# Performance work log

Hardware: AMD Instinct MI355X
Metric: run time of the kernel (lower is better)

The kernel has to match this reference:

```python
import jax, jax.numpy as jnp
import numpy as np

K = 20  # neighbors


def _knn_idx(x, k):
    # x: (B, N, C). pairwise_distance[b,i,j] = -||x_i - x_j||^2; topk -> k nearest (incl. self)
    inner = jnp.einsum('bic,bjc->bij', x, x)            # (B, N, N)
    sq = jnp.sum(x * x, axis=-1)                         # (B, N)
    pd = 2.0 * inner - sq[:, :, None] - sq[:, None, :]   # (B, N, N)
    return jax.lax.top_k(pd, k)[1]                       # (B, N, k) int32


def _gather_neighbors(x, idx):
    # Faithful to source: flatten to (B*N, C) and index with per-batch indices in [0, N).
    # This means every batch gathers from batch 0's rows (bug in original, reproduced).
    B, N, C = x.shape
    flat = x.reshape(B * N, C)
    return flat[idx.reshape(-1)].reshape(B, N, idx.shape[-1], C)  # (B, N, k, C)


def setup_inputs() -> dict:
    key = jax.random.key(0)
    ks = jax.random.split(key, 11)
    B, N = 8, 4096
    emb_dim = 1024
    s = 0.05
    inp = {
        'x':  jax.random.normal(ks[0], (B, N, 3), dtype=jnp.float32),
        'w1': jax.random.normal(ks[1], (3, 64), dtype=jnp.float32) * s,
        'b1': jax.random.normal(ks[2], (64,), dtype=jnp.float32) * s,
        'w2': jax.random.normal(ks[3], (64, 64), dtype=jnp.float32) * s,
        'b2': jax.random.normal(ks[4], (64,), dtype=jnp.float32) * s,
        'w3': jax.random.normal(ks[5], (64, 64), dtype=jnp.float32) * s,
        'b3': jax.random.normal(ks[6], (64,), dtype=jnp.float32) * s,
        'w4': jax.random.normal(ks[7], (64, 128), dtype=jnp.float32) * s,
        'b4': jax.random.normal(ks[8], (128,), dtype=jnp.float32) * s,
        'w5': jax.random.normal(ks[9], (128, emb_dim), dtype=jnp.float32) * s,
        'b5': jax.random.normal(ks[10], (emb_dim,), dtype=jnp.float32) * s,
    }
    return inp


def reference(x, w1, b1, w2, b2, w3, b3, w4, b4, w5, b5):
    # Stage 1: knn on xyz, gather, mlp1 (3->64->64->64 with ReLUs), max over k
    idx = _knn_idx(x, K)                                  # (B, N, K)
    nb = _gather_neighbors(x, idx)                        # (B, N, K, 3)
    h = jax.nn.relu(nb @ w1 + b1)
    h = jax.nn.relu(h @ w2 + b2)
    h = h @ w3 + b3                                       # (B, N, K, 64)
    h = jnp.max(h, axis=2)                                # (B, N, 64)
    # Stage 2: knn on 64-d features, gather, mlp2 (64->128), max over k
    idx = _knn_idx(h, K)
    nb = _gather_neighbors(h, idx)                        # (B, N, K, 64)
    h = nb @ w4 + b4                                      # (B, N, K, 128)
    h = jnp.max(h, axis=2)                                # (B, N, 128)
    # mlp3 (128 -> emb_dim)
    return h @ w5 + b5                                    # (B, N, emb_dim)
```

## Files before the change

kernel.cpp:

```cpp
#include <hip/hip_runtime.h>
#include <stddef.h>

#define NBATCH 8
#define NP 4096
#define KNN 20
#define NEGF (-3.402823466e38f)


template<int G>
__device__ __forceinline__ void knn1_group(const float* __restrict__ xb,
                                           const float* __restrict__ sqb,
                                           int lane, float xi0, float xi1, float xi2,
                                           unsigned mask8, float& gmv, int& gmt) {
  const float* xg = xb + 3 * ((lane << 6) | (G * 8));
  const float* sg = sqb + ((lane << 6) | (G * 8));
  float4 v0 = *(const float4*)(xg + 0);
  float4 v1 = *(const float4*)(xg + 4);
  float4 v2 = *(const float4*)(xg + 8);
  float4 v3 = *(const float4*)(xg + 12);
  float4 v4 = *(const float4*)(xg + 16);
  float4 v5 = *(const float4*)(xg + 20);
  float4 s0 = *(const float4*)(sg + 0);
  float4 s1 = *(const float4*)(sg + 4);
  float d0 = fmaf(xi2, v0.z, fmaf(xi1, v0.y, xi0 * v0.x)); d0 = fmaf(d0, 2.f, -s0.x);
  float d1 = fmaf(xi2, v1.y, fmaf(xi1, v1.x, xi0 * v0.w)); d1 = fmaf(d1, 2.f, -s0.y);
  float d2 = fmaf(xi2, v2.x, fmaf(xi1, v1.w, xi0 * v1.z)); d2 = fmaf(d2, 2.f, -s0.z);
  float d3 = fmaf(xi2, v2.w, fmaf(xi1, v2.z, xi0 * v2.y)); d3 = fmaf(d3, 2.f, -s0.w);
  float d4 = fmaf(xi2, v3.z, fmaf(xi1, v3.y, xi0 * v3.x)); d4 = fmaf(d4, 2.f, -s1.x);
  float d5 = fmaf(xi2, v4.y, fmaf(xi1, v4.x, xi0 * v3.w)); d5 = fmaf(d5, 2.f, -s1.y);
  float d6 = fmaf(xi2, v5.x, fmaf(xi1, v4.w, xi0 * v4.z)); d6 = fmaf(d6, 2.f, -s1.z);
  float d7 = fmaf(xi2, v5.w, fmaf(xi1, v5.z, xi0 * v5.y)); d7 = fmaf(d7, 2.f, -s1.w);
  if (mask8 & 1u)   d0 = NEGF;
  if (mask8 & 2u)   d1 = NEGF;
  if (mask8 & 4u)   d2 = NEGF;
  if (mask8 & 8u)   d3 = NEGF;
  if (mask8 & 16u)  d4 = NEGF;
  if (mask8 & 32u)  d5 = NEGF;
  if (mask8 & 64u)  d6 = NEGF;
  if (mask8 & 128u) d7 = NEGF;
  float mv = d0; int mt = 0;
  if (d1 > mv) { mv = d1; mt = 1; }
  if (d2 > mv) { mv = d2; mt = 2; }
  if (d3 > mv) { mv = d3; mt = 3; }
  if (d4 > mv) { mv = d4; mt = 4; }
  if (d5 > mv) { mv = d5; mt = 5; }
  if (d6 > mv) { mv = d6; mt = 6; }
  if (d7 > mv) { mv = d7; mt = 7; }
  gmv = mv; gmt = G * 8 + mt;
}

template<int G>
__device__ __forceinline__ void sel_group(const float* __restrict__ prow,
                                          unsigned mask8, float& gmv, int& gmt) {
  float4 a = *(const float4*)(prow + G * 8);
  float4 b = *(const float4*)(prow + G * 8 + 4);
  float d0 = a.x, d1 = a.y, d2 = a.z, d3 = a.w;
  float d4 = b.x, d5 = b.y, d6 = b.z, d7 = b.w;
  if (mask8 & 1u)   d0 = NEGF;
  if (mask8 & 2u)   d1 = NEGF;
  if (mask8 & 4u)   d2 = NEGF;
  if (mask8 & 8u)   d3 = NEGF;
  if (mask8 & 16u)  d4 = NEGF;
  if (mask8 & 32u)  d5 = NEGF;
  if (mask8 & 64u)  d6 = NEGF;
  if (mask8 & 128u) d7 = NEGF;
  float mv = d0; int mt = 0;
  if (d1 > mv) { mv = d1; mt = 1; }
  if (d2 > mv) { mv = d2; mt = 2; }
  if (d3 > mv) { mv = d3; mt = 3; }
  if (d4 > mv) { mv = d4; mt = 4; }
  if (d5 > mv) { mv = d5; mt = 5; }
  if (d6 > mv) { mv = d6; mt = 6; }
  if (d7 > mv) { mv = d7; mt = 7; }
  gmv = mv; gmt = G * 8 + mt;
}

#define LANE_SCAN()                                            \
  lv = gv0; lt = gt0;                                          \
  if (gv1 > lv) { lv = gv1; lt = gt1; }                        \
  if (gv2 > lv) { lv = gv2; lt = gt2; }                        \
  if (gv3 > lv) { lv = gv3; lt = gt3; }                        \
  if (gv4 > lv) { lv = gv4; lt = gt4; }                        \
  if (gv5 > lv) { lv = gv5; lt = gt5; }                        \
  if (gv6 > lv) { lv = gv6; lt = gt6; }                        \
  if (gv7 > lv) { lv = gv7; lt = gt7; }

__global__ __launch_bounds__(256) void sq_kernel(const float* __restrict__ x,
                                                 float* __restrict__ sqx) {
  int gid = blockIdx.x * 256 + threadIdx.x;
  float a = x[gid * 3 + 0];
  float b = x[gid * 3 + 1];
  float c = x[gid * 3 + 2];
  sqx[gid] = a * a + b * b + c * c;
}

__global__ __launch_bounds__(256) void knn1_kernel(const float* __restrict__ x,
                                                   const float* __restrict__ sqx,
                                                   int* __restrict__ idx1) {
  int wave = threadIdx.x >> 6, lane = threadIdx.x & 63;
  int row = blockIdx.x * 4 + wave;
  int b = row >> 12;
  int i = row & (NP - 1);
  const float* xb = x + (size_t)b * NP * 3;
  const float* sqb = sqx + b * NP;
  float xi0 = xb[i * 3 + 0], xi1 = xb[i * 3 + 1], xi2 = xb[i * 3 + 2];

  float gv0, gv1, gv2, gv3, gv4, gv5, gv6, gv7;
  int   gt0, gt1, gt2, gt3, gt4, gt5, gt6, gt7;
  unsigned rm0 = 0u, rm1 = 0u;
  knn1_group<0>(xb, sqb, lane, xi0, xi1, xi2, 0u, gv0, gt0);
  knn1_group<1>(xb, sqb, lane, xi0, xi1, xi2, 0u, gv1, gt1);
  knn1_group<2>(xb, sqb, lane, xi0, xi1, xi2, 0u, gv2, gt2);
  knn1_group<3>(xb, sqb, lane, xi0, xi1, xi2, 0u, gv3, gt3);
  knn1_group<4>(xb, sqb, lane, xi0, xi1, xi2, 0u, gv4, gt4);
  knn1_group<5>(xb, sqb, lane, xi0, xi1, xi2, 0u, gv5, gt5);
  knn1_group<6>(xb, sqb, lane, xi0, xi1, xi2, 0u, gv6, gt6);
  knn1_group<7>(xb, sqb, lane, xi0, xi1, xi2, 0u, gv7, gt7);
  float lv; int lt;
  LANE_SCAN();

  int myidx = 0;
  #pragma unroll 1
  for (int r = 0; r < KNN; ++r) {
    float mv = lv;
    int mj = (lane << 6) | lt;
    #pragma unroll
    for (int off = 32; off; off >>= 1) {
      float om = __shfl_xor(mv, off, 64);
      int   oj = __shfl_xor(mj, off, 64);
      if (om > mv || (om == mv && oj < mj)) { mv = om; mj = oj; }
    }
    if (lane == r) myidx = mj;
    int mju = __builtin_amdgcn_readfirstlane(mj);
    int wl = mju >> 6, tu = mju & 63;
    if (lane == wl) {
      switch (tu >> 3) {
        case 0: rm0 |= 1u << (tu & 7);        knn1_group<0>(xb, sqb, lane, xi0, xi1, xi2, rm0 & 0xffu,         gv0, gt0); break;
        case 1: rm0 |= 1u << (8 + (tu & 7));  knn1_group<1>(xb, sqb, lane, xi0, xi1, xi2, (rm0 >> 8) & 0xffu,  gv1, gt1); break;
        case 2: rm0 |= 1u << (16 + (tu & 7)); knn1_group<2>(xb, sqb, lane, xi0, xi1, xi2, (rm0 >> 16) & 0xffu, gv2, gt2); break;
        case 3: rm0 |= 1u << (24 + (tu & 7)); knn1_group<3>(xb, sqb, lane, xi0, xi1, xi2, (rm0 >> 24) & 0xffu, gv3, gt3); break;
        case 4: rm1 |= 1u << (tu & 7);        knn1_group<4>(xb, sqb, lane, xi0, xi1, xi2, rm1 & 0xffu,         gv4, gt4); break;
        case 5: rm1 |= 1u << (8 + (tu & 7));  knn1_group<5>(xb, sqb, lane, xi0, xi1, xi2, (rm1 >> 8) & 0xffu,  gv5, gt5); break;
        case 6: rm1 |= 1u << (16 + (tu & 7)); knn1_group<6>(xb, sqb, lane, xi0, xi1, xi2, (rm1 >> 16) & 0xffu, gv6, gt6); break;
        case 7: rm1 |= 1u << (24 + (tu & 7)); knn1_group<7>(xb, sqb, lane, xi0, xi1, xi2, (rm1 >> 24) & 0xffu, gv7, gt7); break;
      }
      LANE_SCAN();
    }
  }
  if (lane < KNN) idx1[(size_t)row * KNN + lane] = myidx;
}

__global__ __launch_bounds__(256) void mlp1_kernel(const float* __restrict__ x,
                                                   const float* __restrict__ w1, const float* __restrict__ b1,
                                                   const float* __restrict__ w2, const float* __restrict__ b2,
                                                   const float* __restrict__ w3, const float* __restrict__ b3,
                                                   float* __restrict__ F1) {
  int wave = threadIdx.x >> 6, lane = threadIdx.x & 63;
  int j = blockIdx.x * 4 + wave;
  float x0 = x[j * 3 + 0], x1 = x[j * 3 + 1], x2 = x[j * 3 + 2];
  float h1 = fmaf(x2, w1[128 + lane], fmaf(x1, w1[64 + lane], fmaf(x0, w1[lane], b1[lane])));
  h1 = fmaxf(h1, 0.f);
  float acc = b2[lane];
  #pragma unroll
  for (int c = 0; c < 64; ++c) acc = fmaf(__shfl(h1, c, 64), w2[c * 64 + lane], acc);
  float h2 = fmaxf(acc, 0.f);
  acc = b3[lane];
  #pragma unroll
  for (int c = 0; c < 64; ++c) acc = fmaf(__shfl(h2, c, 64), w3[c * 64 + lane], acc);
  F1[j * 64 + lane] = acc;
}

__global__ __launch_bounds__(256) void pool1_kernel(const float* __restrict__ F1,
                                                    const int* __restrict__ idx1,
                                                    float* __restrict__ h,
                                                    float* __restrict__ sqh) {
  int wave = threadIdx.x >> 6, lane = threadIdx.x & 63;
  int row = blockIdx.x * 4 + wave;
  float m = NEGF;
  #pragma unroll
  for (int k = 0; k < KNN; ++k) {
    int jj = idx1[(size_t)row * KNN + k];
    m = fmaxf(m, F1[jj * 64 + lane]);
  }
  h[(size_t)row * 64 + lane] = m;
  float s = m * m;
  #pragma unroll
  for (int off = 32; off; off >>= 1) s += __shfl_xor(s, off, 64);
  if (lane == 0) sqh[row] = s;
}

__device__ __forceinline__ int swz(int g, int r) { return g ^ ((r & 15) ^ ((r >> 4) & 3)); }

__global__ __launch_bounds__(256) void pd_gemm_kernel(const float* __restrict__ h,
                                                      const float* __restrict__ sqh,
                                                      float* __restrict__ pd, int b) {
  __shared__ float As[64 * 64];
  __shared__ float Bs[64 * 64];
  const int it = blockIdx.x >> 6;
  const int jt = blockIdx.x & 63;
  const int i0 = it * 64, j0 = jt * 64;
  const float* hb = h + (size_t)b * NP * 64;
  const int tid = threadIdx.x;
  #pragma unroll
  for (int s = 0; s < 4; ++s) {
    int f4 = tid + s * 256;
    int r = f4 >> 4, g = f4 & 15;
    int gs = swz(g, r);
    float4 va = *reinterpret_cast<const float4*>(&hb[(size_t)(i0 + r) * 64 + g * 4]);
    *reinterpret_cast<float4*>(&As[r * 64 + gs * 4]) = va;
    float4 vb = *reinterpret_cast<const float4*>(&hb[(size_t)(j0 + r) * 64 + g * 4]);
    *reinterpret_cast<float4*>(&Bs[r * 64 + gs * 4]) = vb;
  }
  __syncthreads();
  const int tx = tid & 15, ty = tid >> 4;
  float acc[4][4] = {};
  #pragma unroll
  for (int c = 0; c < 64; c += 4) {
    int g = c >> 2;
    float4 a[4], bb[4];
    #pragma unroll
    for (int q = 0; q < 4; ++q) {
      int r = ty * 4 + q;
      a[q] = *reinterpret_cast<const float4*>(&As[r * 64 + (swz(g, r) << 2)]);
    }
    #pragma unroll
    for (int p = 0; p < 4; ++p) {
      int r = tx * 4 + p;
      bb[p] = *reinterpret_cast<const float4*>(&Bs[r * 64 + (swz(g, r) << 2)]);
    }
    #pragma unroll
    for (int q = 0; q < 4; ++q) {
      #pragma unroll
      for (int p = 0; p < 4; ++p) {
        acc[q][p] = fmaf(a[q].x, bb[p].x, acc[q][p]);
        acc[q][p] = fmaf(a[q].y, bb[p].y, acc[q][p]);
        acc[q][p] = fmaf(a[q].z, bb[p].z, acc[q][p]);
        acc[q][p] = fmaf(a[q].w, bb[p].w, acc[q][p]);
      }
    }
  }
  const float* sq = sqh + b * NP;
  float sj0 = sq[j0 + tx * 4 + 0];
  float sj1 = sq[j0 + tx * 4 + 1];
  float sj2 = sq[j0 + tx * 4 + 2];
  float sj3 = sq[j0 + tx * 4 + 3];
  #pragma unroll
  for (int q = 0; q < 4; ++q) {
    int i = i0 + ty * 4 + q;
    float sqi = sq[i];
    float4 o;
    o.x = 2.f * acc[q][0] - sqi - sj0;
    o.y = 2.f * acc[q][1] - sqi - sj1;
    o.z = 2.f * acc[q][2] - sqi - sj2;
    o.w = 2.f * acc[q][3] - sqi - sj3;
    *reinterpret_cast<float4*>(&pd[(size_t)i * NP + j0 + tx * 4]) = o;
  }
}

__global__ __launch_bounds__(256) void knn_select_kernel(const float* __restrict__ pd,
                                                         int* __restrict__ idx2, int b) {
  int wave = threadIdx.x >> 6, lane = threadIdx.x & 63;
  int row = blockIdx.x * 4 + wave;
  const float* prow = pd + (size_t)row * NP + (lane << 6);

  float gv0, gv1, gv2, gv3, gv4, gv5, gv6, gv7;
  int   gt0, gt1, gt2, gt3, gt4, gt5, gt6, gt7;
  unsigned rm0 = 0u, rm1 = 0u;
  sel_group<0>(prow, 0u, gv0, gt0);
  sel_group<1>(prow, 0u, gv1, gt1);
  sel_group<2>(prow, 0u, gv2, gt2);
  sel_group<3>(prow, 0u, gv3, gt3);
  sel_group<4>(prow, 0u, gv4, gt4);
  sel_group<5>(prow, 0u, gv5, gt5);
  sel_group<6>(prow, 0u, gv6, gt6);
  sel_group<7>(prow, 0u, gv7, gt7);
  float lv; int lt;
  LANE_SCAN();

  int myidx = 0;
  #pragma unroll 1
  for (int r = 0; r < KNN; ++r) {
    float mv = lv;
    int mj = (lane << 6) | lt;
    #pragma unroll
    for (int off = 32; off; off >>= 1) {
      float om = __shfl_xor(mv, off, 64);
      int   oj = __shfl_xor(mj, off, 64);
      if (om > mv || (om == mv && oj < mj)) { mv = om; mj = oj; }
    }
    if (lane == r) myidx = mj;
    int mju = __builtin_amdgcn_readfirstlane(mj);
    int wl = mju >> 6, tu = mju & 63;
    if (lane == wl) {
      switch (tu >> 3) {
        case 0: rm0 |= 1u << (tu & 7);        sel_group<0>(prow, rm0 & 0xffu,         gv0, gt0); break;
        case 1: rm0 |= 1u << (8 + (tu & 7));  sel_group<1>(prow, (rm0 >> 8) & 0xffu,  gv1, gt1); break;
        case 2: rm0 |= 1u << (16 + (tu & 7)); sel_group<2>(prow, (rm0 >> 16) & 0xffu, gv2, gt2); break;
        case 3: rm0 |= 1u << (24 + (tu & 7)); sel_group<3>(prow, (rm0 >> 24) & 0xffu, gv3, gt3); break;
        case 4: rm1 |= 1u << (tu & 7);        sel_group<4>(prow, rm1 & 0xffu,         gv4, gt4); break;
        case 5: rm1 |= 1u << (8 + (tu & 7));  sel_group<5>(prow, (rm1 >> 8) & 0xffu,  gv5, gt5); break;
        case 6: rm1 |= 1u << (16 + (tu & 7)); sel_group<6>(prow, (rm1 >> 16) & 0xffu, gv6, gt6); break;
        case 7: rm1 |= 1u << (24 + (tu & 7)); sel_group<7>(prow, (rm1 >> 24) & 0xffu, gv7, gt7); break;
      }
      LANE_SCAN();
    }
  }
  if (lane < KNN) idx2[(size_t)(b * NP + row) * KNN + lane] = myidx;
}

__device__ __forceinline__ void clear_slot_fb(float (&val)[64], int tw, int lw, int lane) {
  switch (tw) {
#define CS(T) case T: if (lane == lw) val[T] = NEGF; break;
    CS(0) CS(1) CS(2) CS(3) CS(4) CS(5) CS(6) CS(7)
    CS(8) CS(9) CS(10) CS(11) CS(12) CS(13) CS(14) CS(15)
    CS(16) CS(17) CS(18) CS(19) CS(20) CS(21) CS(22) CS(23)
    CS(24) CS(25) CS(26) CS(27) CS(28) CS(29) CS(30) CS(31)
    CS(32) CS(33) CS(34) CS(35) CS(36) CS(37) CS(38) CS(39)
    CS(40) CS(41) CS(42) CS(43) CS(44) CS(45) CS(46) CS(47)
    CS(48) CS(49) CS(50) CS(51) CS(52) CS(53) CS(54) CS(55)
    CS(56) CS(57) CS(58) CS(59) CS(60) CS(61) CS(62) CS(63)
#undef CS
  }
}

__device__ __forceinline__ void wave_topk_fb(float (&val)[64], int lane, int rowbase,
                                             int* __restrict__ idx_out) {
  int myidx = 0;
  #pragma unroll 1
  for (int r = 0; r < KNN; ++r) {
    float m[4]; int mt[4];
    #pragma unroll
    for (int q = 0; q < 4; ++q) { m[q] = val[q]; mt[q] = q; }
    #pragma unroll
    for (int t = 4; t < 64; t += 4) {
      #pragma unroll
      for (int q = 0; q < 4; ++q) {
        if (val[t + q] > m[q]) { m[q] = val[t + q]; mt[q] = t + q; }
      }
    }
    if (m[1] > m[0] || (m[1] == m[0] && mt[1] < mt[0])) { m[0] = m[1]; mt[0] = mt[1]; }
    if (m[3] > m[2] || (m[3] == m[2] && mt[3] < mt[2])) { m[2] = m[3]; mt[2] = mt[3]; }
    if (m[2] > m[0] || (m[2] == m[0] && mt[2] < mt[0])) { m[0] = m[2]; mt[0] = mt[2]; }
    float mv = m[0];
    int mj = mt[0] * 64 + lane;
    #pragma unroll
    for (int off = 32; off; off >>= 1) {
      float om = __shfl_xor(mv, off, 64);
      int   oj = __shfl_xor(mj, off, 64);
      if (om > mv || (om == mv && oj < mj)) { mv = om; mj = oj; }
    }
    clear_slot_fb(val, mj >> 6, mj & 63, lane);
    if (lane == r) myidx = mj;
  }
  if (lane < KNN) idx_out[(size_t)rowbase * KNN + lane] = myidx;
}

__global__ __launch_bounds__(512) void knn2_fused_kernel(const float* __restrict__ h,
                                                         const float* __restrict__ sqh,
                                                         int* __restrict__ idx2) {
  __shared__ float tile[64 * 64];
  const int wave = threadIdx.x >> 6, lane = threadIdx.x & 63;
  const int row = blockIdx.x * 8 + wave;
  const int b = row >> 12;
  const int jb = b * NP;
  float hi[64];
  #pragma unroll
  for (int q2 = 0; q2 < 16; ++q2) {
    float4 v = *reinterpret_cast<const float4*>(&h[(size_t)row * 64 + q2 * 4]);
    hi[q2 * 4 + 0] = v.x; hi[q2 * 4 + 1] = v.y; hi[q2 * 4 + 2] = v.z; hi[q2 * 4 + 3] = v.w;
  }
  float sqi = sqh[row];
  float val[64];
  #pragma unroll
  for (int tt = 0; tt < 64; ++tt) {
    __syncthreads();
    #pragma unroll
    for (int s = 0; s < 2; ++s) {
      int f4 = threadIdx.x + s * 512;
      int jj = f4 >> 4, g = f4 & 15;
      float4 v = *reinterpret_cast<const float4*>(&h[(size_t)(jb + tt * 64 + jj) * 64 + g * 4]);
      int gs = g ^ (jj & 15);
      *reinterpret_cast<float4*>(&tile[jj * 64 + gs * 4]) = v;
    }
    __syncthreads();
    float acc = 0.f;
    #pragma unroll
    for (int g = 0; g < 16; ++g) {
      int gs = g ^ (lane & 15);
      float4 v = *reinterpret_cast<const float4*>(&tile[lane * 64 + gs * 4]);
      acc = fmaf(hi[4 * g + 0], v.x, acc);
      acc = fmaf(hi[4 * g + 1], v.y, acc);
      acc = fmaf(hi[4 * g + 2], v.z, acc);
      acc = fmaf(hi[4 * g + 3], v.w, acc);
    }
    val[tt] = 2.f * acc - sqi - sqh[jb + tt * 64 + lane];
  }
  wave_topk_fb(val, lane, row, idx2);
}

__global__ __launch_bounds__(128) void g4_kernel(const float* __restrict__ h,
                                                 const float* __restrict__ w4,
                                                 const float* __restrict__ b4,
                                                 float* __restrict__ G4) {
  __shared__ float hj[64];
  int j = blockIdx.x;
  int o = threadIdx.x;
  if (o < 64) hj[o] = h[(size_t)j * 64 + o];
  __syncthreads();
  float acc = b4[o];
  #pragma unroll
  for (int c = 0; c < 64; ++c) acc = fmaf(hj[c], w4[c * 128 + o], acc);
  G4[(size_t)j * 128 + o] = acc;
}

__global__ __launch_bounds__(256) void pool2_kernel(const float* __restrict__ G4,
                                                    const int* __restrict__ idx2,
                                                    float* __restrict__ h2) {
  int gid = blockIdx.x * 256 + threadIdx.x;
  int row = gid >> 7, o = gid & 127;
  float m = NEGF;
  #pragma unroll
  for (int k = 0; k < KNN; ++k) {
    int jj = idx2[(size_t)row * KNN + k];
    m = fmaxf(m, G4[(size_t)jj * 128 + o]);
  }
  h2[(size_t)gid] = m;
}

__global__ __launch_bounds__(256) void final_gemm_kernel(const float* __restrict__ h2,
                                                         const float* __restrict__ w5,
                                                         const float* __restrict__ b5,
                                                         float* __restrict__ out) {
  __shared__ float As[64 * 128];
  __shared__ float Bs[128 * 64];
  const int mt = blockIdx.x >> 4;
  const int nt = blockIdx.x & 15;
  const int row0 = mt * 64, col0 = nt * 64;
  const int tid = threadIdx.x;
  #pragma unroll
  for (int s = 0; s < 8; ++s) {
    int f4 = tid + s * 256;
    int i = f4 >> 5, kf = f4 & 31;
    float4 v = *reinterpret_cast<const float4*>(&h2[(size_t)(row0 + i) * 128 + kf * 4]);
    *reinterpret_cast<float4*>(&As[i * 128 + kf * 4]) = v;
  }
  #pragma unroll
  for (int s = 0; s < 8; ++s) {
    int f4 = tid + s * 256;
    int k = f4 >> 4, g = f4 & 15;
    float4 v = *reinterpret_cast<const float4*>(&w5[(size_t)k * 1024 + col0 + g * 4]);
    *reinterpret_cast<float4*>(&Bs[k * 64 + g * 4]) = v;
  }
  __syncthreads();
  const int tx = tid & 15, ty = tid >> 4;
  float acc[4][4] = {};
  #pragma unroll
  for (int k = 0; k < 128; k += 4) {
    float4 a[4], bb[4];
    #pragma unroll
    for (int q = 0; q < 4; ++q)
      a[q] = *reinterpret_cast<const float4*>(&As[(ty * 4 + q) * 128 + k]);
    #pragma unroll
    for (int kk = 0; kk < 4; ++kk)
      bb[kk] = *reinterpret_cast<const float4*>(&Bs[(k + kk) * 64 + tx * 4]);
    #pragma unroll
    for (int q = 0; q < 4; ++q) {
      acc[q][0] = fmaf(a[q].w, bb[3].x, fmaf(a[q].z, bb[2].x, fmaf(a[q].y, bb[1].x, fmaf(a[q].x, bb[0].x, acc[q][0]))));
      acc[q][1] = fmaf(a[q].w, bb[3].y, fmaf(a[q].z, bb[2].y, fmaf(a[q].y, bb[1].y, fmaf(a[q].x, bb[0].y, acc[q][1]))));
      acc[q][2] = fmaf(a[q].w, bb[3].z, fmaf(a[q].z, bb[2].z, fmaf(a[q].y, bb[1].z, fmaf(a[q].x, bb[0].z, acc[q][2]))));
      acc[q][3] = fmaf(a[q].w, bb[3].w, fmaf(a[q].z, bb[2].w, fmaf(a[q].y, bb[1].w, fmaf(a[q].x, bb[0].w, acc[q][3]))));
    }
  }
  float b0 = b5[col0 + tx * 4 + 0];
  float b1 = b5[col0 + tx * 4 + 1];
  float b2 = b5[col0 + tx * 4 + 2];
  float b3 = b5[col0 + tx * 4 + 3];
  #pragma unroll
  for (int q = 0; q < 4; ++q) {
    float4 o;
    o.x = acc[q][0] + b0;
    o.y = acc[q][1] + b1;
    o.z = acc[q][2] + b2;
    o.w = acc[q][3] + b3;
    *reinterpret_cast<float4*>(&out[(size_t)(row0 + ty * 4 + q) * 1024 + col0 + tx * 4]) = o;
  }
}

extern "C" void kernel_launch(void* const* d_in, const int* in_sizes, int n_in,
                              void* d_out, int out_size, void* d_ws, size_t ws_size,
                              hipStream_t stream) {
  const float* x  = (const float*)d_in[0];
  const float* w1 = (const float*)d_in[1];
  const float* b1 = (const float*)d_in[2];
  const float* w2 = (const float*)d_in[3];
  const float* b2 = (const float*)d_in[4];
  const float* w3 = (const float*)d_in[5];
  const float* b3 = (const float*)d_in[6];
  const float* w4 = (const float*)d_in[7];
  const float* b4 = (const float*)d_in[8];
  const float* w5 = (const float*)d_in[9];
  const float* b5 = (const float*)d_in[10];
  float* out = (float*)d_out;
  char* ws = (char*)d_ws;

  float* h    = (float*)(ws + 0);
  float* sqh  = (float*)(ws + 8388608);
  int*   idx2 = (int*)  (ws + 8519680);
  char*  X    = ws + 11141120;
  float* sqx  = (float*)(X + 0);
  int*   idx1 = (int*)  (X + 131072);
  float* F1   = (float*)(X + 2752512);
  float* pd   = (float*)(X + 0);
  float* G4   = (float*)(X + 0);
  float* h2   = (float*)(X + 2097152);

  const size_t NEED_FAST = 11141120 + 67108864;

  sq_kernel<<<128, 256, 0, stream>>>(x, sqx);
  knn1_kernel<<<8192, 256, 0, stream>>>(x, sqx, idx1);
  mlp1_kernel<<<1024, 256, 0, stream>>>(x, w1, b1, w2, b2, w3, b3, F1);
  pool1_kernel<<<8192, 256, 0, stream>>>(F1, idx1, h, sqh);

  if (ws_size >= NEED_FAST) {
    for (int b = 0; b < NBATCH; ++b) {
      pd_gemm_kernel<<<4096, 256, 0, stream>>>(h, sqh, pd, b);
      knn_select_kernel<<<1024, 256, 0, stream>>>(pd, idx2, b);
    }
  } else {
    knn2_fused_kernel<<<4096, 512, 0, stream>>>(h, sqh, idx2);
  }

  g4_kernel<<<4096, 128, 0, stream>>>(h, w4, b4, G4);
  pool2_kernel<<<16384, 256, 0, stream>>>(G4, idx2, h2);
  final_gemm_kernel<<<8192, 256, 0, stream>>>(h2, w5, b5, out);
}
```

Before: 1.182 ms.

## Batch pairwise-distance and select kernels across all batches; use DPP wave max

Adds a path that, when the workspace is large enough, computes the pairwise-distance matrices for all 8 batches in one launch and runs top-k selection for all rows in a second launch. This replaces the 16 per-batch launches and their small-grid tails. Separately, the per-round argmax in both top-k loops becomes a DPP float max plus a ballot and readlane, replacing the shuffle-based value/index butterfly. The batched path needs 512MB of workspace and writes all distance matrices to memory, so it only runs if the harness provides that much.

```diff
diff --git a/kernel.cpp b/kernel.cpp
--- a/kernel.cpp
+++ b/kernel.cpp
@@ -5,6 +5,23 @@
 #define NP 4096
 #define KNN 20
 #define NEGF (-3.402823466e38f)
+
+__device__ __forceinline__ float wave_max_f32(float v) {
+  int b = __float_as_int(v), t;
+  t = __builtin_amdgcn_update_dpp(b, b, 0xB1, 0xf, 0xf, false);
+  b = __float_as_int(fmaxf(__int_as_float(b), __int_as_float(t)));
+  t = __builtin_amdgcn_update_dpp(b, b, 0x4E, 0xf, 0xf, false);
+  b = __float_as_int(fmaxf(__int_as_float(b), __int_as_float(t)));
+  t = __builtin_amdgcn_update_dpp(b, b, 0x124, 0xf, 0xf, false);
+  b = __float_as_int(fmaxf(__int_as_float(b), __int_as_float(t)));
+  t = __builtin_amdgcn_update_dpp(b, b, 0x128, 0xf, 0xf, false);
+  b = __float_as_int(fmaxf(__int_as_float(b), __int_as_float(t)));
+  t = __builtin_amdgcn_update_dpp(b, b, 0x142, 0xa, 0xf, false);
+  b = __float_as_int(fmaxf(__int_as_float(b), __int_as_float(t)));
+  t = __builtin_amdgcn_update_dpp(b, b, 0x143, 0xc, 0xf, false);
+  b = __float_as_int(fmaxf(__int_as_float(b), __int_as_float(t)));
+  return __int_as_float(__builtin_amdgcn_readlane(b, 63));
+}
 
 
 template<int G>
@@ -122,27 +139,21 @@
   int myidx = 0;
   #pragma unroll 1
   for (int r = 0; r < KNN; ++r) {
-    float mv = lv;
-    int mj = (lane << 6) | lt;
-    #pragma unroll
-    for (int off = 32; off; off >>= 1) {
-      float om = __shfl_xor(mv, off, 64);
-      int   oj = __shfl_xor(mj, off, 64);
-      if (om > mv || (om == mv && oj < mj)) { mv = om; mj = oj; }
-    }
-    if (lane == r) myidx = mj;
-    int mju = __builtin_amdgcn_readfirstlane(mj);
-    int wl = mju >> 6, tu = mju & 63;
+    float m = wave_max_f32(lv);
+    unsigned long long bal = __ballot(lv == m);
+    int wl = (int)__builtin_ctzll(bal);
+    int tsel = __builtin_amdgcn_readlane(lt, wl);
+    if (lane == r) myidx = (wl << 6) | tsel;
     if (lane == wl) {
-      switch (tu >> 3) {
-        case 0: rm0 |= 1u << (tu & 7);        knn1_group<0>(xb, sqb, lane, xi0, xi1, xi2, rm0 & 0xffu,         gv0, gt0); break;
-        case 1: rm0 |= 1u << (8 + (tu & 7));  knn1_group<1>(xb, sqb, lane, xi0, xi1, xi2, (rm0 >> 8) & 0xffu,  gv1, gt1); break;
-        case 2: rm0 |= 1u << (16 + (tu & 7)); knn1_group<2>(xb, sqb, lane, xi0, xi1, xi2, (rm0 >> 16) & 0xffu, gv2, gt2); break;
-        case 3: rm0 |= 1u << (24 + (tu & 7)); knn1_group<3>(xb, sqb, lane, xi0, xi1, xi2, (rm0 >> 24) & 0xffu, gv3, gt3); break;
-        case 4: rm1 |= 1u << (tu & 7);        knn1_group<4>(xb, sqb, lane, xi0, xi1, xi2, rm1 & 0xffu,         gv4, gt4); break;
-        case 5: rm1 |= 1u << (8 + (tu & 7));  knn1_group<5>(xb, sqb, lane, xi0, xi1, xi2, (rm1 >> 8) & 0xffu,  gv5, gt5); break;
-        case 6: rm1 |= 1u << (16 + (tu & 7)); knn1_group<6>(xb, sqb, lane, xi0, xi1, xi2, (rm1 >> 16) & 0xffu, gv6, gt6); break;
-        case 7: rm1 |= 1u << (24 + (tu & 7)); knn1_group<7>(xb, sqb, lane, xi0, xi1, xi2, (rm1 >> 24) & 0xffu, gv7, gt7); break;
+      switch (tsel >> 3) {
+        case 0: rm0 |= 1u << (tsel & 7);        knn1_group<0>(xb, sqb, lane, xi0, xi1, xi2, rm0 & 0xffu,         gv0, gt0); break;
+        case 1: rm0 |= 1u << (8 + (tsel & 7));  knn1_group<1>(xb, sqb, lane, xi0, xi1, xi2, (rm0 >> 8) & 0xffu,  gv1, gt1); break;
+        case 2: rm0 |= 1u << (16 + (tsel & 7)); knn1_group<2>(xb, sqb, lane, xi0, xi1, xi2, (rm0 >> 16) & 0xffu, gv2, gt2); break;
+        case 3: rm0 |= 1u << (24 + (tsel & 7)); knn1_group<3>(xb, sqb, lane, xi0, xi1, xi2, (rm0 >> 24) & 0xffu, gv3, gt3); break;
+        case 4: rm1 |= 1u << (tsel & 7);        knn1_group<4>(xb, sqb, lane, xi0, xi1, xi2, rm1 & 0xffu,         gv4, gt4); break;
+        case 5: rm1 |= 1u << (8 + (tsel & 7));  knn1_group<5>(xb, sqb, lane, xi0, xi1, xi2, (rm1 >> 8) & 0xffu,  gv5, gt5); break;
+        case 6: rm1 |= 1u << (16 + (tsel & 7)); knn1_group<6>(xb, sqb, lane, xi0, xi1, xi2, (rm1 >> 16) & 0xffu, gv6, gt6); break;
+        case 7: rm1 |= 1u << (24 + (tsel & 7)); knn1_group<7>(xb, sqb, lane, xi0, xi1, xi2, (rm1 >> 24) & 0xffu, gv7, gt7); break;
       }
       LANE_SCAN();
     }
@@ -150,119 +161,8 @@
   if (lane < KNN) idx1[(size_t)row * KNN + lane] = myidx;
 }
 
-__global__ __launch_bounds__(256) void mlp1_kernel(const float* __restrict__ x,
-                                                   const float* __restrict__ w1, const float* __restrict__ b1,
-                                                   const float* __restrict__ w2, const float* __restrict__ b2,
-                                                   const float* __restrict__ w3, const float* __restrict__ b3,
-                                                   float* __restrict__ F1) {
-  int wave = threadIdx.x >> 6, lane = threadIdx.x & 63;
-  int j = blockIdx.x * 4 + wave;
-  float x0 = x[j * 3 + 0], x1 = x[j * 3 + 1], x2 = x[j * 3 + 2];
-  float h1 = fmaf(x2, w1[128 + lane], fmaf(x1, w1[64 + lane], fmaf(x0, w1[lane], b1[lane])));
-  h1 = fmaxf(h1, 0.f);
-  float acc = b2[lane];
-  #pragma unroll
-  for (int c = 0; c < 64; ++c) acc = fmaf(__shfl(h1, c, 64), w2[c * 64 + lane], acc);
-  float h2 = fmaxf(acc, 0.f);
-  acc = b3[lane];
-  #pragma unroll
-  for (int c = 0; c < 64; ++c) acc = fmaf(__shfl(h2, c, 64), w3[c * 64 + lane], acc);
-  F1[j * 64 + lane] = acc;
-}
-
-__global__ __launch_bounds__(256) void pool1_kernel(const float* __restrict__ F1,
-                                                    const int* __restrict__ idx1,
-                                                    float* __restrict__ h,
-                                                    float* __restrict__ sqh) {
-  int wave = threadIdx.x >> 6, lane = threadIdx.x & 63;
-  int row = blockIdx.x * 4 + wave;
-  float m = NEGF;
-  #pragma unroll
-  for (int k = 0; k < KNN; ++k) {
-    int jj = idx1[(size_t)row * KNN + k];
-    m = fmaxf(m, F1[jj * 64 + lane]);
-  }
-  h[(size_t)row * 64 + lane] = m;
-  float s = m * m;
-  #pragma unroll
-  for (int off = 32; off; off >>= 1) s += __shfl_xor(s, off, 64);
-  if (lane == 0) sqh[row] = s;
-}
-
-__device__ __forceinline__ int swz(int g, int r) { return g ^ ((r & 15) ^ ((r >> 4) & 3)); }
-
-__global__ __launch_bounds__(256) void pd_gemm_kernel(const float* __restrict__ h,
-                                                      const float* __restrict__ sqh,
-                                                      float* __restrict__ pd, int b) {
-  __shared__ float As[64 * 64];
-  __shared__ float Bs[64 * 64];
-  const int it = blockIdx.x >> 6;
-  const int jt = blockIdx.x & 63;
-  const int i0 = it * 64, j0 = jt * 64;
-  const float* hb = h + (size_t)b * NP * 64;
-  const int tid = threadIdx.x;
-  #pragma unroll
-  for (int s = 0; s < 4; ++s) {
-    int f4 = tid + s * 256;
-    int r = f4 >> 4, g = f4 & 15;
-    int gs = swz(g, r);
-    float4 va = *reinterpret_cast<const float4*>(&hb[(size_t)(i0 + r) * 64 + g * 4]);
-    *reinterpret_cast<float4*>(&As[r * 64 + gs * 4]) = va;
-    float4 vb = *reinterpret_cast<const float4*>(&hb[(size_t)(j0 + r) * 64 + g * 4]);
-    *reinterpret_cast<float4*>(&Bs[r * 64 + gs * 4]) = vb;
-  }
-  __syncthreads();
-  const int tx = tid & 15, ty = tid >> 4;
-  float acc[4][4] = {};
-  #pragma unroll
-  for (int c = 0; c < 64; c += 4) {
-    int g = c >> 2;
-    float4 a[4], bb[4];
-    #pragma unroll
-    for (int q = 0; q < 4; ++q) {
-      int r = ty * 4 + q;
-      a[q] = *reinterpret_cast<const float4*>(&As[r * 64 + (swz(g, r) << 2)]);
-    }
-    #pragma unroll
-    for (int p = 0; p < 4; ++p) {
-      int r = tx * 4 + p;
-      bb[p] = *reinterpret_cast<const float4*>(&Bs[r * 64 + (swz(g, r) << 2)]);
-    }
-    #pragma unroll
-    for (int q = 0; q < 4; ++q) {
-      #pragma unroll
-      for (int p = 0; p < 4; ++p) {
-        acc[q][p] = fmaf(a[q].x, bb[p].x, acc[q][p]);
-        acc[q][p] = fmaf(a[q].y, bb[p].y, acc[q][p]);
-        acc[q][p] = fmaf(a[q].z, bb[p].z, acc[q][p]);
-        acc[q][p] = fmaf(a[q].w, bb[p].w, acc[q][p]);
-      }
-    }
-  }
-  const float* sq = sqh + b * NP;
-  float sj0 = sq[j0 + tx * 4 + 0];
-  float sj1 = sq[j0 + tx * 4 + 1];
-  float sj2 = sq[j0 + tx * 4 + 2];
-  float sj3 = sq[j0 + tx * 4 + 3];
-  #pragma unroll
-  for (int q = 0; q < 4; ++q) {
-    int i = i0 + ty * 4 + q;
-    float sqi = sq[i];
-    float4 o;
-    o.x = 2.f * acc[q][0] - sqi - sj0;
-    o.y = 2.f * acc[q][1] - sqi - sj1;
-    o.z = 2.f * acc[q][2] - sqi - sj2;
-    o.w = 2.f * acc[q][3] - sqi - sj3;
-    *reinterpret_cast<float4*>(&pd[(size_t)i * NP + j0 + tx * 4]) = o;
-  }
-}
-
-__global__ __launch_bounds__(256) void knn_select_kernel(const float* __restrict__ pd,
-                                                         int* __restrict__ idx2, int b) {
-  int wave = threadIdx.x >> 6, lane = threadIdx.x & 63;
-  int row = blockIdx.x * 4 + wave;
-  const float* prow = pd + (size_t)row * NP + (lane << 6);
-
+__device__ __forceinline__ void select_row(const float* __restrict__ prow,
+                                           int lane, int* __restrict__ out) {
   float gv0, gv1, gv2, gv3, gv4, gv5, gv6, gv7;
   int   gt0, gt1, gt2, gt3, gt4, gt5, gt6, gt7;
   unsigned rm0 = 0u, rm1 = 0u;
@@ -280,32 +180,161 @@
   int myidx = 0;
   #pragma unroll 1
   for (int r = 0; r < KNN; ++r) {
-    float mv = lv;
-    int mj = (lane << 6) | lt;
-    #pragma unroll
-    for (int off = 32; off; off >>= 1) {
-      float om = __shfl_xor(mv, off, 64);
-      int   oj = __shfl_xor(mj, off, 64);
-      if (om > mv || (om == mv && oj < mj)) { mv = om; mj = oj; }
-    }
-    if (lane == r) myidx = mj;
-    int mju = __builtin_amdgcn_readfirstlane(mj);
-    int wl = mju >> 6, tu = mju & 63;
+    float m = wave_max_f32(lv);
+    unsigned long long bal = __ballot(lv == m);
+    int wl = (int)__builtin_ctzll(bal);
+    int tsel = __builtin_amdgcn_readlane(lt, wl);
+    if (lane == r) myidx = (wl << 6) | tsel;
     if (lane == wl) {
-      switch (tu >> 3) {
-        case 0: rm0 |= 1u << (tu & 7);        sel_group<0>(prow, rm0 & 0xffu,         gv0, gt0); break;
-        case 1: rm0 |= 1u << (8 + (tu & 7));  sel_group<1>(prow, (rm0 >> 8) & 0xffu,  gv1, gt1); break;
-        case 2: rm0 |= 1u << (16 + (tu & 7)); sel_group<2>(prow, (rm0 >> 16) & 0xffu, gv2, gt2); break;
-        case 3: rm0 |= 1u << (24 + (tu & 7)); sel_group<3>(prow, (rm0 >> 24) & 0xffu, gv3, gt3); break;
-        case 4: rm1 |= 1u << (tu & 7);        sel_group<4>(prow, rm1 & 0xffu,         gv4, gt4); break;
-        case 5: rm1 |= 1u << (8 + (tu & 7));  sel_group<5>(prow, (rm1 >> 8) & 0xffu,  gv5, gt5); break;
-        case 6: rm1 |= 1u << (16 + (tu & 7)); sel_group<6>(prow, (rm1 >> 16) & 0xffu, gv6, gt6); break;
-        case 7: rm1 |= 1u << (24 + (tu & 7)); sel_group<7>(prow, (rm1 >> 24) & 0xffu, gv7, gt7); break;
+      switch (tsel >> 3) {
+        case 0: rm0 |= 1u << (tsel & 7);        sel_group<0>(prow, rm0 & 0xffu,         gv0, gt0); break;
+        case 1: rm0 |= 1u << (8 + (tsel & 7));  sel_group<1>(prow, (rm0 >> 8) & 0xffu,  gv1, gt1); break;
+        case 2: rm0 |= 1u << (16 + (tsel & 7)); sel_group<2>(prow, (rm0 >> 16) & 0xffu, gv2, gt2); break;
+        case 3: rm0 |= 1u << (24 + (tsel & 7)); sel_group<3>(prow, (rm0 >> 24) & 0xffu, gv3, gt3); break;
+        case 4: rm1 |= 1u << (tsel & 7);        sel_group<4>(prow, rm1 & 0xffu,         gv4, gt4); break;
+        case 5: rm1 |= 1u << (8 + (tsel & 7));  sel_group<5>(prow, (rm1 >> 8) & 0xffu,  gv5, gt5); break;
+        case 6: rm1 |= 1u << (16 + (tsel & 7)); sel_group<6>(prow, (rm1 >> 16) & 0xffu, gv6, gt6); break;
+        case 7: rm1 |= 1u << (24 + (tsel & 7)); sel_group<7>(prow, (rm1 >> 24) & 0xffu, gv7, gt7); break;
       }
       LANE_SCAN();
     }
   }
-  if (lane < KNN) idx2[(size_t)(b * NP + row) * KNN + lane] = myidx;
+  if (lane < KNN) out[lane] = myidx;
+}
+
+__global__ __launch_bounds__(256) void knn_select_kernel(const float* __restrict__ pd,
+                                                         int* __restrict__ idx2, int b) {
+  int wave = threadIdx.x >> 6, lane = threadIdx.x & 63;
+  int row = blockIdx.x * 4 + wave;
+  select_row(pd + (size_t)row * NP + (lane << 6), lane,
+             idx2 + (size_t)(b * NP + row) * KNN);
+}
+
+__global__ __launch_bounds__(256) void knn_select_all_kernel(const float* __restrict__ pd8,
+                                                             int* __restrict__ idx2) {
+  int wave = threadIdx.x >> 6, lane = threadIdx.x & 63;
+  int rowg = blockIdx.x * 4 + wave;
+  select_row(pd8 + (size_t)rowg * NP + (lane << 6), lane,
+             idx2 + (size_t)rowg * KNN);
+}
+
+__global__ __launch_bounds__(256) void mlp1_kernel(const float* __restrict__ x,
+                                                   const float* __restrict__ w1, const float* __restrict__ b1,
+                                                   const float* __restrict__ w2, const float* __restrict__ b2,
+                                                   const float* __restrict__ w3, const float* __restrict__ b3,
+                                                   float* __restrict__ F1) {
+  int wave = threadIdx.x >> 6, lane = threadIdx.x & 63;
+  int j = blockIdx.x * 4 + wave;
+  float x0 = x[j * 3 + 0], x1 = x[j * 3 + 1], x2 = x[j * 3 + 2];
+  float h1 = fmaf(x2, w1[128 + lane], fmaf(x1, w1[64 + lane], fmaf(x0, w1[lane], b1[lane])));
+  h1 = fmaxf(h1, 0.f);
+  float acc = b2[lane];
+  #pragma unroll
+  for (int c = 0; c < 64; ++c) acc = fmaf(__shfl(h1, c, 64), w2[c * 64 + lane], acc);
+  float h2 = fmaxf(acc, 0.f);
+  acc = b3[lane];
+  #pragma unroll
+  for (int c = 0; c < 64; ++c) acc = fmaf(__shfl(h2, c, 64), w3[c * 64 + lane], acc);
+  F1[j * 64 + lane] = acc;
+}
+
+__global__ __launch_bounds__(256) void pool1_kernel(const float* __restrict__ F1,
+                                                    const int* __restrict__ idx1,
+                                                    float* __restrict__ h,
+                                                    float* __restrict__ sqh) {
+  int wave = threadIdx.x >> 6, lane = threadIdx.x & 63;
+  int row = blockIdx.x * 4 + wave;
+  float m = NEGF;
+  #pragma unroll
+  for (int k = 0; k < KNN; ++k) {
+    int jj = idx1[(size_t)row * KNN + k];
+    m = fmaxf(m, F1[jj * 64 + lane]);
+  }
+  h[(size_t)row * 64 + lane] = m;
+  float s = m * m;
+  #pragma unroll
+  for (int off = 32; off; off >>= 1) s += __shfl_xor(s, off, 64);
+  if (lane == 0) sqh[row] = s;
+}
+
+__device__ __forceinline__ int swz(int g, int r) { return g ^ ((r & 15) ^ ((r >> 4) & 3)); }
+
+__device__ __forceinline__ void pd_tile(const float* __restrict__ hb,
+                                        const float* __restrict__ sq,
+                                        float* __restrict__ pdb,
+                                        int it, int jt, int tid) {
+  __shared__ float As[64 * 64];
+  __shared__ float Bs[64 * 64];
+  const int i0 = it * 64, j0 = jt * 64;
+  #pragma unroll
+  for (int s = 0; s < 4; ++s) {
+    int f4 = tid + s * 256;
+    int r = f4 >> 4, g = f4 & 15;
+    int gs = swz(g, r);
+    float4 va = *reinterpret_cast<const float4*>(&hb[(size_t)(i0 + r) * 64 + g * 4]);
+    *reinterpret_cast<float4*>(&As[r * 64 + gs * 4]) = va;
+    float4 vb = *reinterpret_cast<const float4*>(&hb[(size_t)(j0 + r) * 64 + g * 4]);
+    *reinterpret_cast<float4*>(&Bs[r * 64 + gs * 4]) = vb;
+  }
+  __syncthreads();
+  const int tx = tid & 15, ty = tid >> 4;
+  float acc[4][4] = {};
+  #pragma unroll
+  for (int c = 0; c < 64; c += 4) {
+    int g = c >> 2;
+    float4 a[4], bb[4];
+    #pragma unroll
+    for (int q = 0; q < 4; ++q) {
+      int r = ty * 4 + q;
+      a[q] = *reinterpret_cast<const float4*>(&As[r * 64 + (swz(g, r) << 2)]);
+    }
+    #pragma unroll
+    for (int p = 0; p < 4; ++p) {
+      int r = tx * 4 + p;
+      bb[p] = *reinterpret_cast<const float4*>(&Bs[r * 64 + (swz(g, r) << 2)]);
+    }
+    #pragma unroll
+    for (int q = 0; q < 4; ++q) {
+      #pragma unroll
+      for (int p = 0; p < 4; ++p) {
+        acc[q][p] = fmaf(a[q].x, bb[p].x, acc[q][p]);
+        acc[q][p] = fmaf(a[q].y, bb[p].y, acc[q][p]);
+        acc[q][p] = fmaf(a[q].z, bb[p].z, acc[q][p]);
+        acc[q][p] = fmaf(a[q].w, bb[p].w, acc[q][p]);
+      }
+    }
+  }
+  float sj0 = sq[j0 + tx * 4 + 0];
+  float sj1 = sq[j0 + tx * 4 + 1];
+  float sj2 = sq[j0 + tx * 4 + 2];
+  float sj3 = sq[j0 + tx * 4 + 3];
+  #pragma unroll
+  for (int q = 0; q < 4; ++q) {
+    int i = i0 + ty * 4 + q;
+    float sqi = sq[i];
+    float4 o;
+    o.x = 2.f * acc[q][0] - sqi - sj0;
+    o.y = 2.f * acc[q][1] - sqi - sj1;
+    o.z = 2.f * acc[q][2] - sqi - sj2;
+    o.w = 2.f * acc[q][3] - sqi - sj3;
+    *reinterpret_cast<float4*>(&pdb[(size_t)i * NP + j0 + tx * 4]) = o;
+  }
+}
+
+__global__ __launch_bounds__(256) void pd_gemm_kernel(const float* __restrict__ h,
+                                                      const float* __restrict__ sqh,
+                                                      float* __restrict__ pd, int b) {
+  pd_tile(h + (size_t)b * NP * 64, sqh + b * NP, pd,
+          blockIdx.x >> 6, blockIdx.x & 63, threadIdx.x);
+}
+
+__global__ __launch_bounds__(256) void pd_gemm_all_kernel(const float* __restrict__ h,
+                                                          const float* __restrict__ sqh,
+                                                          float* __restrict__ pd8) {
+  int b = blockIdx.x >> 12;
+  int tile = blockIdx.x & 4095;
+  pd_tile(h + (size_t)b * NP * 64, sqh + b * NP, pd8 + (size_t)b * NP * NP,
+          tile >> 6, tile & 63, threadIdx.x);
 }
 
 __device__ __forceinline__ void clear_slot_fb(float (&val)[64], int tw, int lw, int lane) {
@@ -514,14 +543,19 @@
   float* G4   = (float*)(X + 0);
   float* h2   = (float*)(X + 2097152);
 
-  const size_t NEED_FAST = 11141120 + 67108864;
+  const size_t OVERLAY   = 11141120;
+  const size_t NEED_FAST = OVERLAY + (size_t)NP * NP * 4;
+  const size_t NEED_FULL = OVERLAY + (size_t)NBATCH * NP * NP * 4;
 
   sq_kernel<<<128, 256, 0, stream>>>(x, sqx);
   knn1_kernel<<<8192, 256, 0, stream>>>(x, sqx, idx1);
   mlp1_kernel<<<1024, 256, 0, stream>>>(x, w1, b1, w2, b2, w3, b3, F1);
   pool1_kernel<<<8192, 256, 0, stream>>>(F1, idx1, h, sqh);
 
-  if (ws_size >= NEED_FAST) {
+  if (ws_size >= NEED_FULL) {
+    pd_gemm_all_kernel<<<32768, 256, 0, stream>>>(h, sqh, pd);
+    knn_select_all_kernel<<<8192, 256, 0, stream>>>(pd, idx2);
+  } else if (ws_size >= NEED_FAST) {
     for (int b = 0; b < NBATCH; ++b) {
       pd_gemm_kernel<<<4096, 256, 0, stream>>>(h, sqh, pd, b);
       knn_select_kernel<<<1024, 256, 0, stream>>>(pd, idx2, b);
```

After: 1.023 ms. 13.5% less time.
